# Kernel optimization log

Measured on AMD Instinct MI355X. Metric: run time of the kernel, lower is better.

The kernel has to match this reference:

```python
import jax, jax.numpy as jnp
import numpy as np

B, S, H = 1, 2048, 4096
N_HEADS, N_KV, HEAD_DIM = 32, 8, 128
ROPE_THETA = 10000.0


def setup_inputs() -> dict:
    key = jax.random.key(0)
    k1, k2, k3 = jax.random.split(key, 3)
    hidden_states = jax.random.normal(k1, (B, S, H), dtype=jnp.float32)
    # fused QKV projection weight: rows = (n_heads + 2*n_kv_heads) * head_dim
    Wqkv = jax.random.normal(k2, ((N_HEADS + 2 * N_KV) * HEAD_DIM, H), dtype=jnp.float32) * 0.02
    Wo = jax.random.normal(k3, (H, N_HEADS * HEAD_DIM), dtype=jnp.float32) * 0.02
    return {"hidden_states": hidden_states, "Wqkv": Wqkv, "Wo": Wo}


def _rope_tables(seqlen, dim, theta):
    inv_freq = 1.0 / (theta ** (jnp.arange(0, dim, 2, dtype=jnp.float32) / dim))  # [dim/2]
    t = jnp.arange(seqlen, dtype=jnp.float32)
    freqs = jnp.outer(t, inv_freq)  # [S, dim/2]
    return jnp.cos(freqs), jnp.sin(freqs)


def _apply_rope(x, cos, sin):
    # torch code: reshape(...,2,-1).transpose -> view_as_complex pairs (x[j], x[j+d/2])
    # i.e. NeoX rotate-half on first/second halves of head_dim.
    d2 = x.shape[-1] // 2
    x1, x2 = x[..., :d2], x[..., d2:]
    c = cos[None, :, None, :]  # [1,S,1,d/2]
    s = sin[None, :, None, :]
    return jnp.concatenate([x1 * c - x2 * s, x1 * s + x2 * c], axis=-1)


def reference(hidden_states, Wqkv, Wo):
    b, s, h = hidden_states.shape
    # fused QKV projection
    qkv = jnp.einsum('bsh,oh->bso', hidden_states, Wqkv)
    q_end = N_HEADS * HEAD_DIM
    k_end = q_end + N_KV * HEAD_DIM
    xq = qkv[..., :q_end].reshape(b, s, N_HEADS, HEAD_DIM)
    xk = qkv[..., q_end:k_end].reshape(b, s, N_KV, HEAD_DIM)
    xv = qkv[..., k_end:].reshape(b, s, N_KV, HEAD_DIM)
    # RoPE (start_pos = 0 prefill)
    cos, sin = _rope_tables(s, HEAD_DIM, ROPE_THETA)
    xq = _apply_rope(xq, cos, sin)
    xk = _apply_rope(xk, cos, sin)
    # GQA: expand kv heads to query heads (head h uses kv head h // groups)
    groups = N_HEADS // N_KV
    xk = jnp.repeat(xk, groups, axis=2)  # [b,s,nH,hd]
    xv = jnp.repeat(xv, groups, axis=2)
    # causal attention, softmax scale 1/sqrt(head_dim) (flash_attn default, softcap=0)
    scale = 1.0 / jnp.sqrt(jnp.float32(HEAD_DIM))
    scores = jnp.einsum('bqhd,bkhd->bhqk', xq, xk) * scale
    causal = jnp.tril(jnp.ones((s, s), dtype=bool))
    scores = jnp.where(causal[None, None, :, :], scores, jnp.float32(-1e30))
    probs = jax.nn.softmax(scores, axis=-1)
    out = jnp.einsum('bhqk,bkhd->bqhd', probs, xv).reshape(b, s, N_HEADS * HEAD_DIM)
    attn_output = jnp.einsum('bsd,hd->bsh', out, Wo)
    return attn_output
```

## Files before the change

### kernel.cpp

```cpp
#include <hip/hip_runtime.h>
#include <stdint.h>

typedef unsigned short u16;
typedef unsigned int   u32;
typedef short bf16x8 __attribute__((ext_vector_type(8)));
typedef float f32x4  __attribute__((ext_vector_type(4)));

__device__ __forceinline__ u16 f2bf(float f) {
    union { float f; u32 u; } v; v.f = f;
    u32 u = v.u;
    u32 r = (u + 0x7fffu + ((u >> 16) & 1u)) >> 16;
    return (u16)r;
}
__device__ __forceinline__ float bf2f(u16 h) {
    union { u32 u; float f; } v; v.u = ((u32)h) << 16;
    return v.f;
}

__device__ __forceinline__ void gload_lds16(const void* g, void* l) {
    __builtin_amdgcn_global_load_lds(
        (__attribute__((address_space(1))) void*)g,
        (__attribute__((address_space(3))) void*)l,
        16, 0, 0);
}

__global__ __launch_bounds__(256) void cvt_bf16(const float4* __restrict__ s,
                                                uint2* __restrict__ d, int n4) {
    int i = blockIdx.x * 256 + threadIdx.x;
    if (i < n4) {
        float4 v = s[i];
        uint2 o;
        o.x = (u32)f2bf(v.x) | ((u32)f2bf(v.y) << 16);
        o.y = (u32)f2bf(v.z) | ((u32)f2bf(v.w) << 16);
        d[i] = o;
    }
}

template <typename OUT_T>
__global__ __launch_bounds__(256) void gemm_bt(const u16* __restrict__ A,
                                               const u16* __restrict__ B,
                                               OUT_T* __restrict__ C,
                                               int M, int N, int K) {
    __shared__ u16 As[128 * 32];
    __shared__ u16 Bs[128 * 32];

    const int tid  = threadIdx.x;
    const int lane = tid & 63;
    const int wv   = tid >> 6;
    const int row0 = blockIdx.y * 128;
    const int col0 = blockIdx.x * 128;

    const int wm = (wv >> 1) * 64;
    const int wn = (wv & 1) * 64;
    const int fr = lane & 15;
    const int fq = (lane >> 4) * 8;

    const int srow = lane >> 2;
    const int scol = (lane & 3) * 8;

    f32x4 acc[4][4];
#pragma unroll
    for (int i = 0; i < 4; ++i)
#pragma unroll
        for (int j = 0; j < 4; ++j) acc[i][j] = f32x4{0.f, 0.f, 0.f, 0.f};

    for (int k0 = 0; k0 < K; k0 += 32) {
        __syncthreads();
#pragma unroll
        for (int i = 0; i < 2; ++i) {
            const int chunk = wv * 2 + i;
            const int r     = chunk * 16 + srow;
            gload_lds16(A + (size_t)(row0 + r) * K + k0 + scol, &As[r * 32 + scol]);
            gload_lds16(B + (size_t)(col0 + r) * K + k0 + scol, &Bs[r * 32 + scol]);
        }
        __syncthreads();

        bf16x8 af[4], bf[4];
#pragma unroll
        for (int mt = 0; mt < 4; ++mt)
            af[mt] = *(const bf16x8*)&As[(wm + mt * 16 + fr) * 32 + fq];
#pragma unroll
        for (int nt = 0; nt < 4; ++nt)
            bf[nt] = *(const bf16x8*)&Bs[(wn + nt * 16 + fr) * 32 + fq];
#pragma unroll
        for (int mt = 0; mt < 4; ++mt)
#pragma unroll
            for (int nt = 0; nt < 4; ++nt)
                acc[mt][nt] = __builtin_amdgcn_mfma_f32_16x16x32_bf16(
                    af[mt], bf[nt], acc[mt][nt], 0, 0, 0);
    }

    const int orow4 = (lane >> 4) * 4;
    const int ocol  = lane & 15;
#pragma unroll
    for (int mt = 0; mt < 4; ++mt)
#pragma unroll
        for (int nt = 0; nt < 4; ++nt)
#pragma unroll
            for (int r = 0; r < 4; ++r) {
                int mm = row0 + wm + mt * 16 + orow4 + r;
                int nn = col0 + wn + nt * 16 + ocol;
                float v = acc[mt][nt][r];
                if constexpr (sizeof(OUT_T) == 2)
                    C[(size_t)mm * N + nn] = (OUT_T)f2bf(v);
                else
                    C[(size_t)mm * N + nn] = (OUT_T)v;
            }
}

__global__ __launch_bounds__(256) void rope_scatter(const u16* __restrict__ qkv,
                                                    u16* __restrict__ Qb,
                                                    u16* __restrict__ Kb) {
    int id = blockIdx.x * 256 + threadIdx.x;
    int d    = id & 63;
    int t    = id >> 6;
    int head = t % 40;
    int s    = t / 40;

    const size_t rowbase = (size_t)s * 6144;
    float inv = __expf(-(float)d * (9.210340371976184f / 64.0f));
    float ang = (float)s * inv;
    float cs, sn; __sincosf(ang, &sn, &cs);

    if (head < 32) {
        float x1 = bf2f(qkv[rowbase + head * 128 + d]);
        float x2 = bf2f(qkv[rowbase + head * 128 + d + 64]);
        size_t o = ((size_t)head * 2048 + s) * 128 + d;
        Qb[o]      = f2bf(x1 * cs - x2 * sn);
        Qb[o + 64] = f2bf(x1 * sn + x2 * cs);
    } else {
        int kh = head - 32;
        float x1 = bf2f(qkv[rowbase + 4096 + kh * 128 + d]);
        float x2 = bf2f(qkv[rowbase + 4096 + kh * 128 + d + 64]);
        size_t o = ((size_t)kh * 2048 + s) * 128 + d;
        Kb[o]      = f2bf(x1 * cs - x2 * sn);
        Kb[o + 64] = f2bf(x1 * sn + x2 * cs);
    }
}

__global__ __launch_bounds__(256) void transpose_v(const u16* __restrict__ qkv,
                                                   u16* __restrict__ Vt) {
    int id = blockIdx.x * 256 + threadIdx.x;
    int s8 = id & 255;
    int d  = (id >> 8) & 127;
    int vh = id >> 15;
    u16 tmp[8];
#pragma unroll
    for (int j = 0; j < 8; ++j)
        tmp[j] = qkv[(size_t)(s8 * 8 + j) * 6144 + 5120 + vh * 128 + d];
    *(uint4*)(Vt + ((size_t)vh * 128 + d) * 2048 + s8 * 8) = *(uint4*)tmp;
}

__global__ __launch_bounds__(256) void attn_mfma(const u16* __restrict__ Qb,
                                                 const u16* __restrict__ Kb,
                                                 const u16* __restrict__ Vt,
                                                 u16* __restrict__ ctx) {
    __shared__ u16 Ks[64 * 128];
    __shared__ u16 Vs[128 * 64];
    __shared__ u16 Ps[4][16 * 72];

    const int tid  = threadIdx.x;
    const int lane = tid & 63;
    const int w    = tid >> 6;
    const int m    = lane & 15;
    const int quad = lane >> 4;
    const int h    = blockIdx.y;
    const int kh   = h >> 2;

    const u16* Ktile0 = Kb + (size_t)kh * 2048 * 128;
    const u16* Vtile0 = Vt + (size_t)kh * 128 * 2048;
    const float sl2e = 0.08838834764831845f * 1.4426950408889634f;

    for (int rep = 0; rep < 2; ++rep) {
        const int qt = rep ? (31 - blockIdx.x) : blockIdx.x;

        bf16x8 qf[4];
        {
            const u16* qp = Qb + ((size_t)h * 2048 + qt * 64 + w * 16 + m) * 128 + quad * 8;
#pragma unroll
            for (int kk = 0; kk < 4; ++kk)
                qf[kk] = *(const bf16x8*)(qp + kk * 32);
        }

        f32x4 acc[8];
#pragma unroll
        for (int i = 0; i < 8; ++i) acc[i] = f32x4{0.f, 0.f, 0.f, 0.f};
        float lr[4] = {0.f, 0.f, 0.f, 0.f};

        for (int kt = 0; kt <= qt; ++kt) {
            __syncthreads();
            {
                const u16* Kt = Ktile0 + (size_t)kt * 64 * 128;
#pragma unroll
                for (int i = 0; i < 4; ++i) {
                    int slot = i * 256 + tid;
                    int row = slot >> 4, cp = slot & 15;
                    int gc = cp ^ (row & 7);
                    gload_lds16(Kt + row * 128 + gc * 8, &Ks[slot * 8]);
                }
                const u16* Vtt = Vtile0 + kt * 64;
#pragma unroll
                for (int i = 0; i < 4; ++i) {
                    int slot = i * 256 + tid;
                    int row = slot >> 3, cp = slot & 7;
                    int gc = cp ^ (row & 7);
                    gload_lds16(Vtt + (size_t)row * 2048 + gc * 8, &Vs[slot * 8]);
                }
            }
            __syncthreads();

            f32x4 sacc[4];
#pragma unroll
            for (int nt = 0; nt < 4; ++nt) sacc[nt] = f32x4{0.f, 0.f, 0.f, 0.f};
#pragma unroll
            for (int kk = 0; kk < 4; ++kk) {
#pragma unroll
                for (int nt = 0; nt < 4; ++nt) {
                    int pos = (kk * 4 + quad) ^ (m & 7);
                    bf16x8 b = *(const bf16x8*)&Ks[(nt * 16 + m) * 128 + pos * 8];
                    sacc[nt] = __builtin_amdgcn_mfma_f32_16x16x32_bf16(qf[kk], b, sacc[nt], 0, 0, 0);
                }
            }

            const bool diag = (kt == qt);
            float ls[4] = {0.f, 0.f, 0.f, 0.f};
#pragma unroll
            for (int nt = 0; nt < 4; ++nt)
#pragma unroll
                for (int r = 0; r < 4; ++r) {
                    float p = __builtin_amdgcn_exp2f(sacc[nt][r] * sl2e);
                    if (diag && (nt * 16 + m > w * 16 + quad * 4 + r)) p = 0.f;
                    sacc[nt][r] = p;
                    ls[r] += p;
                }
#pragma unroll
            for (int r = 0; r < 4; ++r) lr[r] += ls[r];

#pragma unroll
            for (int nt = 0; nt < 4; ++nt)
#pragma unroll
                for (int r = 0; r < 4; ++r)
                    Ps[w][(quad * 4 + r) * 72 + nt * 16 + m] = f2bf(sacc[nt][r]);

#pragma unroll
            for (int kk2 = 0; kk2 < 2; ++kk2) {
                bf16x8 a = *(const bf16x8*)&Ps[w][m * 72 + kk2 * 32 + quad * 8];
#pragma unroll
                for (int nt = 0; nt < 8; ++nt) {
                    int n = nt * 16 + m;
                    int pos = (kk2 * 4 + quad) ^ (m & 7);
                    bf16x8 b = *(const bf16x8*)&Vs[n * 64 + pos * 8];
                    acc[nt] = __builtin_amdgcn_mfma_f32_16x16x32_bf16(a, b, acc[nt], 0, 0, 0);
                }
            }
        }

#pragma unroll
        for (int r = 0; r < 4; ++r) {
            float s_ = lr[r];
            s_ += __shfl_xor(s_, 1);
            s_ += __shfl_xor(s_, 2);
            s_ += __shfl_xor(s_, 4);
            s_ += __shfl_xor(s_, 8);
            lr[r] = s_;
        }

#pragma unroll
        for (int r = 0; r < 4; ++r) {
            float inv = 1.f / lr[r];
            size_t rowg = (size_t)(qt * 64 + w * 16 + quad * 4 + r);
#pragma unroll
            for (int nt = 0; nt < 8; ++nt)
                ctx[rowg * 4096 + h * 128 + nt * 16 + m] = f2bf(acc[nt][r] * inv);
        }
    }
}

extern "C" void kernel_launch(void* const* d_in, const int* in_sizes, int n_in,
                              void* d_out, int out_size, void* d_ws, size_t ws_size,
                              hipStream_t stream) {
    const float* hs   = (const float*)d_in[0];
    const float* wqkv = (const float*)d_in[1];
    const float* wo   = (const float*)d_in[2];
    float* out = (float*)d_out;

    char* ws = (char*)d_ws;
    u16* hA  = (u16*)ws;  ws += (size_t)2048 * 4096 * 2;
    u16* wQ  = (u16*)ws;  ws += (size_t)6144 * 4096 * 2;
    u16* wO  = (u16*)ws;  ws += (size_t)4096 * 4096 * 2;
    u16* qkv = (u16*)ws;  ws += (size_t)2048 * 6144 * 2;
    u16* Qb  = (u16*)ws;  ws += (size_t)32 * 2048 * 128 * 2;
    u16* Kb  = (u16*)ws;  ws += (size_t)8 * 2048 * 128 * 2;
    u16* Vt  = (u16*)ws;  ws += (size_t)8 * 128 * 2048 * 2;
    u16* ctx = (u16*)ws;  ws += (size_t)2048 * 4096 * 2;

    cvt_bf16<<<8192, 256, 0, stream>>>((const float4*)hs,   (uint2*)hA, 2048 * 4096 / 4);
    cvt_bf16<<<24576, 256, 0, stream>>>((const float4*)wqkv, (uint2*)wQ, 6144 * 4096 / 4);
    cvt_bf16<<<16384, 256, 0, stream>>>((const float4*)wo,   (uint2*)wO, 4096 * 4096 / 4);

    gemm_bt<u16><<<dim3(48, 16), 256, 0, stream>>>(hA, wQ, qkv, 2048, 6144, 4096);

    rope_scatter<<<20480, 256, 0, stream>>>(qkv, Qb, Kb);
    transpose_v<<<1024, 256, 0, stream>>>(qkv, Vt);

    attn_mfma<<<dim3(16, 32), 256, 0, stream>>>(Qb, Kb, Vt, ctx);

    gemm_bt<float><<<dim3(32, 16), 256, 0, stream>>>(ctx, wO, out, 2048, 4096, 4096);
}
```

Before: 552.1 us.

## Fuse Q RoPE into attention, share K/V tiles across paired query tiles

Merges the three fp32->bf16 conversion launches into one kernel and combines K RoPE with the V transpose into a single prep kernel. Q RoPE now runs in the attention prologue straight from the qkv buffer, so the Qb intermediate buffer and its write/read traffic go away. Each attention block processes its two query tiles (qt and 31-qt) in one shared KV loop, loading each K/V tile once instead of twice. The cost is roughly doubled accumulator register use, which may lower occupancy, plus per-element sincos work in the attention prologue.

```diff
diff --git a/kernel.cpp b/kernel.cpp
--- a/kernel.cpp
+++ b/kernel.cpp
@@ -24,16 +24,19 @@
         16, 0, 0);
 }
 
-__global__ __launch_bounds__(256) void cvt_bf16(const float4* __restrict__ s,
-                                                uint2* __restrict__ d, int n4) {
-    int i = blockIdx.x * 256 + threadIdx.x;
-    if (i < n4) {
-        float4 v = s[i];
-        uint2 o;
-        o.x = (u32)f2bf(v.x) | ((u32)f2bf(v.y) << 16);
-        o.y = (u32)f2bf(v.z) | ((u32)f2bf(v.w) << 16);
-        d[i] = o;
-    }
+__global__ __launch_bounds__(256) void cvt_all(const float4* __restrict__ s1, uint2* __restrict__ d1,
+                                               const float4* __restrict__ s2, uint2* __restrict__ d2,
+                                               const float4* __restrict__ s3, uint2* __restrict__ d3) {
+    const float4* s; uint2* d; int i;
+    int b = blockIdx.x;
+    if (b < 8192)        { s = s1; d = d1; i = b * 256 + threadIdx.x; }
+    else if (b < 32768)  { s = s2; d = d2; i = (b - 8192) * 256 + threadIdx.x; }
+    else                 { s = s3; d = d3; i = (b - 32768) * 256 + threadIdx.x; }
+    float4 v = s[i];
+    uint2 o;
+    o.x = (u32)f2bf(v.x) | ((u32)f2bf(v.y) << 16);
+    o.y = (u32)f2bf(v.z) | ((u32)f2bf(v.w) << 16);
+    d[i] = o;
 }
 
 template <typename OUT_T>
@@ -108,50 +111,83 @@
             }
 }
 
-__global__ __launch_bounds__(256) void rope_scatter(const u16* __restrict__ qkv,
-                                                    u16* __restrict__ Qb,
-                                                    u16* __restrict__ Kb) {
-    int id = blockIdx.x * 256 + threadIdx.x;
-    int d    = id & 63;
-    int t    = id >> 6;
-    int head = t % 40;
-    int s    = t / 40;
-
-    const size_t rowbase = (size_t)s * 6144;
-    float inv = __expf(-(float)d * (9.210340371976184f / 64.0f));
-    float ang = (float)s * inv;
-    float cs, sn; __sincosf(ang, &sn, &cs);
-
-    if (head < 32) {
-        float x1 = bf2f(qkv[rowbase + head * 128 + d]);
-        float x2 = bf2f(qkv[rowbase + head * 128 + d + 64]);
-        size_t o = ((size_t)head * 2048 + s) * 128 + d;
-        Qb[o]      = f2bf(x1 * cs - x2 * sn);
-        Qb[o + 64] = f2bf(x1 * sn + x2 * cs);
-    } else {
-        int kh = head - 32;
-        float x1 = bf2f(qkv[rowbase + 4096 + kh * 128 + d]);
-        float x2 = bf2f(qkv[rowbase + 4096 + kh * 128 + d + 64]);
+__global__ __launch_bounds__(256) void prep_kv(const u16* __restrict__ qkv,
+                                               u16* __restrict__ Kb,
+                                               u16* __restrict__ Vt) {
+    if (blockIdx.x < 4096) {
+        int id = blockIdx.x * 256 + threadIdx.x;
+        int d  = id & 63;
+        int t  = id >> 6;
+        int kh = t & 7;
+        int s  = t >> 3;
+        const size_t rowbase = (size_t)s * 6144 + 4096;
+        float inv = __expf(-(float)d * (9.210340371976184f / 64.0f));
+        float ang = (float)s * inv;
+        float cs, sn; __sincosf(ang, &sn, &cs);
+        float x1 = bf2f(qkv[rowbase + kh * 128 + d]);
+        float x2 = bf2f(qkv[rowbase + kh * 128 + d + 64]);
         size_t o = ((size_t)kh * 2048 + s) * 128 + d;
         Kb[o]      = f2bf(x1 * cs - x2 * sn);
         Kb[o + 64] = f2bf(x1 * sn + x2 * cs);
-    }
-}
-
-__global__ __launch_bounds__(256) void transpose_v(const u16* __restrict__ qkv,
-                                                   u16* __restrict__ Vt) {
-    int id = blockIdx.x * 256 + threadIdx.x;
-    int s8 = id & 255;
-    int d  = (id >> 8) & 127;
-    int vh = id >> 15;
-    u16 tmp[8];
-#pragma unroll
-    for (int j = 0; j < 8; ++j)
-        tmp[j] = qkv[(size_t)(s8 * 8 + j) * 6144 + 5120 + vh * 128 + d];
-    *(uint4*)(Vt + ((size_t)vh * 128 + d) * 2048 + s8 * 8) = *(uint4*)tmp;
-}
-
-__global__ __launch_bounds__(256) void attn_mfma(const u16* __restrict__ Qb,
+    } else {
+        int id = (blockIdx.x - 4096) * 256 + threadIdx.x;
+        int s8 = id & 255;
+        int d  = (id >> 8) & 127;
+        int vh = id >> 15;
+        u16 tmp[8];
+#pragma unroll
+        for (int j = 0; j < 8; ++j)
+            tmp[j] = qkv[(size_t)(s8 * 8 + j) * 6144 + 5120 + vh * 128 + d];
+        *(uint4*)(Vt + ((size_t)vh * 128 + d) * 2048 + s8 * 8) = *(uint4*)tmp;
+    }
+}
+
+__device__ __forceinline__ void attn_pass(const bf16x8 qf[4], f32x4 acc[8], float lr[4],
+                                          const u16* Ks, const u16* Vs, u16* Psw,
+                                          int w, int m, int quad, bool diag, float sl2e) {
+    f32x4 sacc[4];
+#pragma unroll
+    for (int nt = 0; nt < 4; ++nt) sacc[nt] = f32x4{0.f, 0.f, 0.f, 0.f};
+#pragma unroll
+    for (int kk = 0; kk < 4; ++kk) {
+#pragma unroll
+        for (int nt = 0; nt < 4; ++nt) {
+            int pos = (kk * 4 + quad) ^ (m & 7);
+            bf16x8 b = *(const bf16x8*)&Ks[(nt * 16 + m) * 128 + pos * 8];
+            sacc[nt] = __builtin_amdgcn_mfma_f32_16x16x32_bf16(qf[kk], b, sacc[nt], 0, 0, 0);
+        }
+    }
+
+#pragma unroll
+    for (int nt = 0; nt < 4; ++nt)
+#pragma unroll
+        for (int r = 0; r < 4; ++r) {
+            float p = __builtin_amdgcn_exp2f(sacc[nt][r] * sl2e);
+            if (diag && (nt * 16 + m > w * 16 + quad * 4 + r)) p = 0.f;
+            sacc[nt][r] = p;
+            lr[r] += p;
+        }
+
+#pragma unroll
+    for (int nt = 0; nt < 4; ++nt)
+#pragma unroll
+        for (int r = 0; r < 4; ++r)
+            Psw[(quad * 4 + r) * 72 + nt * 16 + m] = f2bf(sacc[nt][r]);
+
+#pragma unroll
+    for (int kk2 = 0; kk2 < 2; ++kk2) {
+        bf16x8 a = *(const bf16x8*)&Psw[m * 72 + kk2 * 32 + quad * 8];
+#pragma unroll
+        for (int nt = 0; nt < 8; ++nt) {
+            int n = nt * 16 + m;
+            int pos = (kk2 * 4 + quad) ^ (m & 7);
+            bf16x8 b = *(const bf16x8*)&Vs[n * 64 + pos * 8];
+            acc[nt] = __builtin_amdgcn_mfma_f32_16x16x32_bf16(a, b, acc[nt], 0, 0, 0);
+        }
+    }
+}
+
+__global__ __launch_bounds__(256) void attn_mfma(const u16* __restrict__ qkv,
                                                  const u16* __restrict__ Kb,
                                                  const u16* __restrict__ Vt,
                                                  u16* __restrict__ ctx) {
@@ -166,95 +202,77 @@
     const int quad = lane >> 4;
     const int h    = blockIdx.y;
     const int kh   = h >> 2;
+    const int qtA  = blockIdx.x;
+    const int qtB  = 31 - qtA;
 
     const u16* Ktile0 = Kb + (size_t)kh * 2048 * 128;
     const u16* Vtile0 = Vt + (size_t)kh * 128 * 2048;
     const float sl2e = 0.08838834764831845f * 1.4426950408889634f;
 
-    for (int rep = 0; rep < 2; ++rep) {
-        const int qt = rep ? (31 - blockIdx.x) : blockIdx.x;
-
-        bf16x8 qf[4];
+    bf16x8 qa[4], qb[4];
+#pragma unroll
+    for (int which = 0; which < 2; ++which) {
+        const int qt = which ? qtB : qtA;
+        const int s  = qt * 64 + w * 16 + m;
+        bf16x8 raw[4];
+        const u16* qp = qkv + (size_t)s * 6144 + h * 128 + quad * 8;
+#pragma unroll
+        for (int kk = 0; kk < 4; ++kk)
+            raw[kk] = *(const bf16x8*)(qp + kk * 32);
+        bf16x8* dst = which ? qb : qa;
+#pragma unroll
+        for (int half = 0; half < 2; ++half)
+#pragma unroll
+            for (int j = 0; j < 8; ++j) {
+                int d = half * 32 + quad * 8 + j;
+                float inv = __expf(-(float)d * (9.210340371976184f / 64.0f));
+                float ang = (float)s * inv;
+                float cs, sn; __sincosf(ang, &sn, &cs);
+                float x1 = bf2f(((const u16*)&raw[half])[j]);
+                float x2 = bf2f(((const u16*)&raw[half + 2])[j]);
+                ((u16*)&dst[half])[j]     = f2bf(x1 * cs - x2 * sn);
+                ((u16*)&dst[half + 2])[j] = f2bf(x1 * sn + x2 * cs);
+            }
+    }
+
+    f32x4 accA[8], accB[8];
+#pragma unroll
+    for (int i = 0; i < 8; ++i) { accA[i] = f32x4{0.f, 0.f, 0.f, 0.f}; accB[i] = f32x4{0.f, 0.f, 0.f, 0.f}; }
+    float lA[4] = {0.f, 0.f, 0.f, 0.f};
+    float lB[4] = {0.f, 0.f, 0.f, 0.f};
+
+    for (int kt = 0; kt <= qtB; ++kt) {
+        __syncthreads();
         {
-            const u16* qp = Qb + ((size_t)h * 2048 + qt * 64 + w * 16 + m) * 128 + quad * 8;
-#pragma unroll
-            for (int kk = 0; kk < 4; ++kk)
-                qf[kk] = *(const bf16x8*)(qp + kk * 32);
-        }
-
-        f32x4 acc[8];
-#pragma unroll
-        for (int i = 0; i < 8; ++i) acc[i] = f32x4{0.f, 0.f, 0.f, 0.f};
-        float lr[4] = {0.f, 0.f, 0.f, 0.f};
-
-        for (int kt = 0; kt <= qt; ++kt) {
-            __syncthreads();
-            {
-                const u16* Kt = Ktile0 + (size_t)kt * 64 * 128;
-#pragma unroll
-                for (int i = 0; i < 4; ++i) {
-                    int slot = i * 256 + tid;
-                    int row = slot >> 4, cp = slot & 15;
-                    int gc = cp ^ (row & 7);
-                    gload_lds16(Kt + row * 128 + gc * 8, &Ks[slot * 8]);
-                }
-                const u16* Vtt = Vtile0 + kt * 64;
-#pragma unroll
-                for (int i = 0; i < 4; ++i) {
-                    int slot = i * 256 + tid;
-                    int row = slot >> 3, cp = slot & 7;
-                    int gc = cp ^ (row & 7);
-                    gload_lds16(Vtt + (size_t)row * 2048 + gc * 8, &Vs[slot * 8]);
-                }
+            const u16* Kt = Ktile0 + (size_t)kt * 64 * 128;
+#pragma unroll
+            for (int i = 0; i < 4; ++i) {
+                int slot = i * 256 + tid;
+                int row = slot >> 4, cp = slot & 15;
+                int gc = cp ^ (row & 7);
+                gload_lds16(Kt + row * 128 + gc * 8, &Ks[slot * 8]);
             }
-            __syncthreads();
-
-            f32x4 sacc[4];
-#pragma unroll
-            for (int nt = 0; nt < 4; ++nt) sacc[nt] = f32x4{0.f, 0.f, 0.f, 0.f};
-#pragma unroll
-            for (int kk = 0; kk < 4; ++kk) {
-#pragma unroll
-                for (int nt = 0; nt < 4; ++nt) {
-                    int pos = (kk * 4 + quad) ^ (m & 7);
-                    bf16x8 b = *(const bf16x8*)&Ks[(nt * 16 + m) * 128 + pos * 8];
-                    sacc[nt] = __builtin_amdgcn_mfma_f32_16x16x32_bf16(qf[kk], b, sacc[nt], 0, 0, 0);
-                }
+            const u16* Vtt = Vtile0 + kt * 64;
+#pragma unroll
+            for (int i = 0; i < 4; ++i) {
+                int slot = i * 256 + tid;
+                int row = slot >> 3, cp = slot & 7;
+                int gc = cp ^ (row & 7);
+                gload_lds16(Vtt + (size_t)row * 2048 + gc * 8, &Vs[slot * 8]);
             }
-
-            const bool diag = (kt == qt);
-            float ls[4] = {0.f, 0.f, 0.f, 0.f};
-#pragma unroll
-            for (int nt = 0; nt < 4; ++nt)
-#pragma unroll
-                for (int r = 0; r < 4; ++r) {
-                    float p = __builtin_amdgcn_exp2f(sacc[nt][r] * sl2e);
-                    if (diag && (nt * 16 + m > w * 16 + quad * 4 + r)) p = 0.f;
-                    sacc[nt][r] = p;
-                    ls[r] += p;
-                }
-#pragma unroll
-            for (int r = 0; r < 4; ++r) lr[r] += ls[r];
-
-#pragma unroll
-            for (int nt = 0; nt < 4; ++nt)
-#pragma unroll
-                for (int r = 0; r < 4; ++r)
-                    Ps[w][(quad * 4 + r) * 72 + nt * 16 + m] = f2bf(sacc[nt][r]);
-
-#pragma unroll
-            for (int kk2 = 0; kk2 < 2; ++kk2) {
-                bf16x8 a = *(const bf16x8*)&Ps[w][m * 72 + kk2 * 32 + quad * 8];
-#pragma unroll
-                for (int nt = 0; nt < 8; ++nt) {
-                    int n = nt * 16 + m;
-                    int pos = (kk2 * 4 + quad) ^ (m & 7);
-                    bf16x8 b = *(const bf16x8*)&Vs[n * 64 + pos * 8];
-                    acc[nt] = __builtin_amdgcn_mfma_f32_16x16x32_bf16(a, b, acc[nt], 0, 0, 0);
-                }
-            }
-        }
-
+        }
+        __syncthreads();
+
+        if (kt <= qtA)
+            attn_pass(qa, accA, lA, Ks, Vs, Ps[w], w, m, quad, kt == qtA, sl2e);
+        attn_pass(qb, accB, lB, Ks, Vs, Ps[w], w, m, quad, kt == qtB, sl2e);
+    }
+
+#pragma unroll
+    for (int which = 0; which < 2; ++which) {
+        const int qt   = which ? qtB : qtA;
+        f32x4*   acc   = which ? accB : accA;
+        float*   lr    = which ? lB   : lA;
 #pragma unroll
         for (int r = 0; r < 4; ++r) {
             float s_ = lr[r];
@@ -264,7 +282,6 @@
             s_ += __shfl_xor(s_, 8);
             lr[r] = s_;
         }
-
 #pragma unroll
         for (int r = 0; r < 4; ++r) {
             float inv = 1.f / lr[r];
@@ -289,21 +306,19 @@
     u16* wQ  = (u16*)ws;  ws += (size_t)6144 * 4096 * 2;
     u16* wO  = (u16*)ws;  ws += (size_t)4096 * 4096 * 2;
     u16* qkv = (u16*)ws;  ws += (size_t)2048 * 6144 * 2;
-    u16* Qb  = (u16*)ws;  ws += (size_t)32 * 2048 * 128 * 2;
     u16* Kb  = (u16*)ws;  ws += (size_t)8 * 2048 * 128 * 2;
     u16* Vt  = (u16*)ws;  ws += (size_t)8 * 128 * 2048 * 2;
     u16* ctx = (u16*)ws;  ws += (size_t)2048 * 4096 * 2;
 
-    cvt_bf16<<<8192, 256, 0, stream>>>((const float4*)hs,   (uint2*)hA, 2048 * 4096 / 4);
-    cvt_bf16<<<24576, 256, 0, stream>>>((const float4*)wqkv, (uint2*)wQ, 6144 * 4096 / 4);
-    cvt_bf16<<<16384, 256, 0, stream>>>((const float4*)wo,   (uint2*)wO, 4096 * 4096 / 4);
+    cvt_all<<<49152, 256, 0, stream>>>((const float4*)hs,   (uint2*)hA,
+                                       (const float4*)wqkv, (uint2*)wQ,
+                                       (const float4*)wo,   (uint2*)wO);
 
     gemm_bt<u16><<<dim3(48, 16), 256, 0, stream>>>(hA, wQ, qkv, 2048, 6144, 4096);
 
-    rope_scatter<<<20480, 256, 0, stream>>>(qkv, Qb, Kb);
-    transpose_v<<<1024, 256, 0, stream>>>(qkv, Vt);
-
-    attn_mfma<<<dim3(16, 32), 256, 0, stream>>>(Qb, Kb, Vt, ctx);
+    prep_kv<<<5120, 256, 0, stream>>>(qkv, Kb, Vt);
+
+    attn_mfma<<<dim3(16, 32), 256, 0, stream>>>(qkv, Kb, Vt, ctx);
 
     gemm_bt<float><<<dim3(32, 16), 256, 0, stream>>>(ctx, wO, out, 2048, 4096, 4096);
 }
```

After: 545.5 us. No clear change (-1.2%).
